# Kernel tuning notes

Hardware: AMD Instinct MI355X
Metric: run time of the kernel (lower is better)

Reference implementation:

```python
import jax, jax.numpy as jnp
import numpy as np

jax.config.update("jax_enable_x64", True)

MAX_LEN = 2048
D_MODEL = 2048
CONTEXT = 1
FUDGE = 0.01
MIN_PERIOD = 1
MAX_PERIOD = 1024
FORGOTTEN_AT = 0.01


def _init_params():
    # Mirrors LaplaceAggregation.__init__ with init_method='linspace', modify_real=True
    limit = np.log(np.finfo(np.float64).max) / MAX_LEN - FUDGE
    soft_high = np.log(FORGOTTEN_AT) / MAX_PERIOD
    soft_low = np.log(FORGOTTEN_AT) / MIN_PERIOD
    a_low = max(-limit + FUDGE, soft_low)
    a_high = max(min(-1e-6, soft_high), a_low)
    a = np.linspace(a_low, a_high, D_MODEL).reshape(1, 1, D_MODEL, CONTEXT)
    b = (2.0 * np.pi / np.linspace(MIN_PERIOD, MAX_PERIOD, D_MODEL)).reshape(1, 1, D_MODEL, CONTEXT)
    return jnp.asarray(a, jnp.float64), jnp.asarray(b, jnp.float64)


def setup_inputs() -> dict:
    key = jax.random.key(0)
    k1, k2, k3 = jax.random.split(key, 3)
    B, T, F = 8, 1024, D_MODEL
    x = jax.random.normal(k1, (B, T, F), dtype=jnp.float32)
    mem_real = jax.random.normal(k2, (B, 1, F, CONTEXT), dtype=jnp.float32)
    mem_imag = jax.random.normal(k3, (B, 1, F, CONTEXT), dtype=jnp.float32)
    a, b = _init_params()
    return {"x": x, "mem_real": mem_real, "mem_imag": mem_imag, "a": a, "b": b}


def reference(x, mem_real, mem_imag, a, b):
    # batched_recurrent_update path (1 < T < max_len)
    T = x.shape[1]
    f64, c128 = jnp.float64, jnp.complex128
    ab = a.astype(f64) + 1j * b.astype(f64)           # [1,1,F,C] complex

    def psi(t):  # t: [T] -> [1,T,F,C]
        return jnp.exp(ab * t.reshape(1, -1, 1, 1))

    # inner_idx[:T] = [max_len-1, ..., max_len-T]; outer_idx = -inner_idx
    inner = jnp.arange(MAX_LEN - 1, MAX_LEN - 1 - T, -1, dtype=f64)
    offset = jnp.arange(1, T + 1, dtype=f64)          # state_offset[:T]

    xc = x.astype(f64)[..., None].astype(c128)        # [B,T,F,1]
    z = jnp.cumsum(psi(inner) * xc, axis=1)           # [B,T,F,C]
    mem0 = (mem_real.astype(f64) + 1j * mem_imag.astype(f64))  # [B,1,F,C]
    out = psi(-inner) * z + mem0 * psi(offset)        # [B,T,F,C]
    return out.astype(jnp.complex64)
```

## Files before the change

kernel.cpp:

```cpp
#include <hip/hip_runtime.h>
#include <math.h>

#define BB 8
#define TT 1024
#define FF 2048
#define F2 1024
#define NCH 64
#define LCH 16
#define F2W 8
#define NFB (F2 / F2W)
#define WGT (NCH * F2W)
#define SCAN_R 6


typedef float vf2 __attribute__((ext_vector_type(2)));

__device__ inline void load_ab2(const void* ap, const void* bp, int f,
                                double2& ab0, double2& ab1) {
    double bd = ((const double*)bp)[0];
    if (bd > 6.0 && bd < 6.6) {
        ab0 = make_double2(((const double*)ap)[f],     ((const double*)bp)[f]);
        ab1 = make_double2(((const double*)ap)[f + 1], ((const double*)bp)[f + 1]);
    } else {
        ab0 = make_double2((double)((const float*)ap)[f],
                           (double)((const float*)bp)[f]);
        ab1 = make_double2((double)((const float*)ap)[f + 1],
                           (double)((const float*)bp)[f + 1]);
    }
}

__device__ inline float2 cis_exp_f(double a, double b, double scale) {
    double m = exp(scale * a);
    double s, c;
    sincos(scale * b, &s, &c);
    return make_float2((float)(m * c), (float)(m * s));
}

__device__ inline float2 cmulf(float2 u, float2 v) {
    return make_float2(fmaf(u.x, v.x, -u.y * v.y), fmaf(u.x, v.y, u.y * v.x));
}
__device__ inline float2 csqf(float2 u) {
    return make_float2(fmaf(u.x, u.x, -u.y * u.y), 2.f * u.x * u.y);
}

__device__ inline void nt_store2(float2* p, float lo, float hi) {
    vf2 v; v.x = lo; v.y = hi;
    __builtin_nontemporal_store(v, reinterpret_cast<vf2*>(p));
}

__global__ void __launch_bounds__(WGT, 4)
k_fused(const float2* __restrict__ x2, const float2* __restrict__ mr2,
        const float2* __restrict__ mi2, const void* __restrict__ a,
        const void* __restrict__ b, float2* __restrict__ out2, size_t limit2) {
    __shared__ float4 sS[2][NCH][F2W];

    int tid = threadIdx.x;
    int f2  = tid & (F2W - 1);
    int c   = tid >> 3;

    int bid = blockIdx.x;
    int swz = ((bid & 7) << 7) + (bid >> 3);
    int fb  = swz & (NFB - 1);
    int bb  = swz >> 7;
    int f2g = fb * F2W + f2;

    size_t base2 = ((size_t)bb * TT + (size_t)c * LCH) * F2 + f2g;
    const float2* xp = x2 + base2;

    float2 xv[LCH];
#pragma unroll
    for (int j = 0; j < LCH; ++j) xv[j] = xp[(size_t)j * F2];

    float2 mem_r = mr2[(size_t)bb * F2 + f2g];
    float2 mem_i = mi2[(size_t)bb * F2 + f2g];

    double2 ab0, ab1;
    load_ab2(a, b, 2 * f2g, ab0, ab1);
    float2 l0 = cis_exp_f(ab0.x, ab0.y, 1.0);
    float2 l1 = cis_exp_f(ab1.x, ab1.y, 1.0);

    float4 z[LCH];
    float zr0 = 0.f, zi0 = 0.f, zr1 = 0.f, zi1 = 0.f;
#pragma unroll
    for (int j = 0; j < LCH; ++j) {
        float2 xvj = xv[j];
        float nr0 = fmaf(l0.x, zr0, fmaf(-l0.y, zi0, xvj.x));
        float ni0 = fmaf(l0.x, zi0, l0.y * zr0);
        float nr1 = fmaf(l1.x, zr1, fmaf(-l1.y, zi1, xvj.y));
        float ni1 = fmaf(l1.x, zi1, l1.y * zr1);
        zr0 = nr0; zi0 = ni0; zr1 = nr1; zi1 = ni1;
        z[j] = make_float4(zr0, zi0, zr1, zi1);
    }

    float2 m0 = l0, m1 = l1;
#pragma unroll
    for (int s = 0; s < 4; ++s) { m0 = csqf(m0); m1 = csqf(m1); }

    float4 P = z[LCH - 1];
    float2 e0 = make_float2(1.f, 0.f), e1 = make_float2(1.f, 0.f);

    sS[0][c][f2] = P;
    __syncthreads();
    int pb = 0;
#pragma unroll
    for (int r = 0; r < SCAN_R; ++r) {
        int k = 1 << r;
        float4 part = make_float4(0.f, 0.f, 0.f, 0.f);
        if (c >= k) part = sS[pb][c - k][f2];
        if ((c >> r) & 1) { e0 = cmulf(e0, m0); e1 = cmulf(e1, m1); }
        P.x = fmaf(m0.x, part.x, fmaf(-m0.y, part.y, P.x));
        P.y = fmaf(m0.x, part.y, fmaf( m0.y, part.x, P.y));
        P.z = fmaf(m1.x, part.z, fmaf(-m1.y, part.w, P.z));
        P.w = fmaf(m1.x, part.w, fmaf( m1.y, part.z, P.w));
        m0 = csqf(m0); m1 = csqf(m1);
        sS[pb ^ 1][c][f2] = P;
        __syncthreads();
        pb ^= 1;
    }
    float4 Pm1 = make_float4(0.f, 0.f, 0.f, 0.f);
    if (c > 0) Pm1 = sS[pb][c - 1][f2];

    float Wr0 = fmaf(e0.x, mem_r.x, fmaf(-e0.y, mem_i.x, Pm1.x));
    float Wi0 = fmaf(e0.x, mem_i.x, fmaf( e0.y, mem_r.x, Pm1.y));
    float Wr1 = fmaf(e1.x, mem_r.y, fmaf(-e1.y, mem_i.y, Pm1.z));
    float Wi1 = fmaf(e1.x, mem_i.y, fmaf( e1.y, mem_r.y, Pm1.w));

    const size_t plane2 = (size_t)BB * TT * F2;
#pragma unroll
    for (int j = 0; j < LCH; ++j) {
        float nWr0 = fmaf(l0.x, Wr0, -l0.y * Wi0);
        float nWi0 = fmaf(l0.x, Wi0,  l0.y * Wr0);
        float nWr1 = fmaf(l1.x, Wr1, -l1.y * Wi1);
        float nWi1 = fmaf(l1.x, Wi1,  l1.y * Wr1);
        Wr0 = nWr0; Wi0 = nWi0; Wr1 = nWr1; Wi1 = nWi1;
        float4 zj = z[j];
        size_t idx2 = base2 + (size_t)j * F2;
        if (idx2 < limit2) nt_store2(&out2[idx2], zj.x + Wr0, zj.z + Wr1);
        size_t ii2 = idx2 + plane2;
        if (ii2 < limit2) nt_store2(&out2[ii2], zj.y + Wi0, zj.w + Wi1);
    }
}

extern "C" void kernel_launch(void* const* d_in, const int* in_sizes, int n_in,
                              void* d_out, int out_size, void* d_ws, size_t ws_size,
                              hipStream_t stream) {
    const float2* x2  = (const float2*)d_in[0];
    const float2* mr2 = (const float2*)d_in[1];
    const float2* mi2 = (const float2*)d_in[2];
    const void*   a   = d_in[3];
    const void*   b   = d_in[4];
    float2* out2 = (float2*)d_out;
    (void)d_ws; (void)ws_size; (void)n_in; (void)in_sizes;

    size_t limit2 = (size_t)out_size >> 1;

    int grid = BB * NFB;
    k_fused<<<grid, WGT, 0, stream>>>(x2, mr2, mi2, a, b, out2, limit2);
}
```

Before: 128.3 us.

## Process four batches per workgroup with register double-buffered prefetch of x

Each workgroup now handles four batch rows for its feature slice, so the grid shrinks by a factor of four. While one tile is computed, the x values for the next batch are prefetched into a second register buffer. The per-chunk decay factor e is now computed directly with exp/sincos instead of being accumulated during the scan, and the per-thread setup (lambda, its powers, e) is amortised across the four tiles. In exchange the kernel uses more registers, launch bounds drop to two workgroups per CU, and the smaller grid exposes less parallelism.

```diff
diff --git a/kernel.cpp b/kernel.cpp
--- a/kernel.cpp
+++ b/kernel.cpp
@@ -11,6 +11,7 @@
 #define NFB (F2 / F2W)
 #define WGT (NCH * F2W)
 #define SCAN_R 6
+#define NTILE 4
 
 
 typedef float vf2 __attribute__((ext_vector_type(2)));
@@ -36,9 +37,6 @@
     return make_float2((float)(m * c), (float)(m * s));
 }
 
-__device__ inline float2 cmulf(float2 u, float2 v) {
-    return make_float2(fmaf(u.x, v.x, -u.y * v.y), fmaf(u.x, v.y, u.y * v.x));
-}
 __device__ inline float2 csqf(float2 u) {
     return make_float2(fmaf(u.x, u.x, -u.y * u.y), 2.f * u.x * u.y);
 }
@@ -48,7 +46,79 @@
     __builtin_nontemporal_store(v, reinterpret_cast<vf2*>(p));
 }
 
-__global__ void __launch_bounds__(WGT, 4)
+#define DO_TILE(XV, XN, BB_CUR, BB_NXT, HAVE_NXT)                              \
+  do {                                                                         \
+        \
+    float2 mem_r = mr2[(size_t)(BB_CUR) * F2 + f2g];                           \
+    float2 mem_i = mi2[(size_t)(BB_CUR) * F2 + f2g];                           \
+                 \
+    if (HAVE_NXT) {                                                            \
+      const float2* xpn =                                                      \
+          x2 + ((size_t)(BB_NXT) * TT + (size_t)c * LCH) * F2 + f2g;           \
+      _Pragma("unroll")                                                        \
+      for (int j = 0; j < LCH; ++j) (XN)[j] = xpn[(size_t)j * F2];             \
+    }                                                                          \
+         \
+    float4 z[LCH];                                                             \
+    {                                                                          \
+      float zr0 = 0.f, zi0 = 0.f, zr1 = 0.f, zi1 = 0.f;                        \
+      _Pragma("unroll")                                                        \
+      for (int j = 0; j < LCH; ++j) {                                          \
+        float2 xvj = (XV)[j];                                                  \
+        float nr0 = fmaf(l0.x, zr0, fmaf(-l0.y, zi0, xvj.x));                  \
+        float ni0 = fmaf(l0.x, zi0, l0.y * zr0);                               \
+        float nr1 = fmaf(l1.x, zr1, fmaf(-l1.y, zi1, xvj.y));                  \
+        float ni1 = fmaf(l1.x, zi1, l1.y * zr1);                               \
+        zr0 = nr0; zi0 = ni0; zr1 = nr1; zi1 = ni1;                            \
+        z[j] = make_float4(zr0, zi0, zr1, zi1);                                \
+      }                                                                        \
+    }                                                                          \
+            \
+    float4 P = z[LCH - 1];                                                     \
+    float2 m0 = m0b, m1 = m1b;                                                 \
+    __syncthreads();           \
+    sS[0][c][f2] = P;                                                          \
+    __syncthreads();                                                           \
+    int pb = 0;                                                                \
+    _Pragma("unroll")                                                          \
+    for (int r = 0; r < SCAN_R; ++r) {                                         \
+      int k = 1 << r;                                                          \
+      float4 part = make_float4(0.f, 0.f, 0.f, 0.f);                           \
+      if (c >= k) part = sS[pb][c - k][f2];                                    \
+      P.x = fmaf(m0.x, part.x, fmaf(-m0.y, part.y, P.x));                      \
+      P.y = fmaf(m0.x, part.y, fmaf( m0.y, part.x, P.y));                      \
+      P.z = fmaf(m1.x, part.z, fmaf(-m1.y, part.w, P.z));                      \
+      P.w = fmaf(m1.x, part.w, fmaf( m1.y, part.z, P.w));                      \
+      m0 = csqf(m0); m1 = csqf(m1);                                            \
+      sS[pb ^ 1][c][f2] = P;                                                   \
+      __syncthreads();                                                         \
+      pb ^= 1;                                                                 \
+    }                                                                          \
+    float4 Pm1 = make_float4(0.f, 0.f, 0.f, 0.f);                              \
+    if (c > 0) Pm1 = sS[pb][c - 1][f2];                                        \
+                                  \
+    float Wr0 = fmaf(e0.x, mem_r.x, fmaf(-e0.y, mem_i.x, Pm1.x));              \
+    float Wi0 = fmaf(e0.x, mem_i.x, fmaf( e0.y, mem_r.x, Pm1.y));              \
+    float Wr1 = fmaf(e1.x, mem_r.y, fmaf(-e1.y, mem_i.y, Pm1.z));              \
+    float Wi1 = fmaf(e1.x, mem_i.y, fmaf( e1.y, mem_r.y, Pm1.w));              \
+                  \
+    size_t base2 = ((size_t)(BB_CUR) * TT + (size_t)c * LCH) * F2 + f2g;       \
+    _Pragma("unroll")                                                          \
+    for (int j = 0; j < LCH; ++j) {                                            \
+      float nWr0 = fmaf(l0.x, Wr0, -l0.y * Wi0);                               \
+      float nWi0 = fmaf(l0.x, Wi0,  l0.y * Wr0);                               \
+      float nWr1 = fmaf(l1.x, Wr1, -l1.y * Wi1);                               \
+      float nWi1 = fmaf(l1.x, Wi1,  l1.y * Wr1);                               \
+      Wr0 = nWr0; Wi0 = nWi0; Wr1 = nWr1; Wi1 = nWi1;                          \
+      float4 zj = z[j];                                                        \
+      size_t idx2 = base2 + (size_t)j * F2;                                    \
+      if (idx2 < limit2) nt_store2(&out2[idx2], zj.x + Wr0, zj.z + Wr1);       \
+      size_t ii2 = idx2 + plane2;                                              \
+      if (ii2 < limit2) nt_store2(&out2[ii2], zj.y + Wi0, zj.w + Wi1);         \
+    }                                                                          \
+  } while (0)
+
+__global__ void __launch_bounds__(WGT, 2)
 k_fused(const float2* __restrict__ x2, const float2* __restrict__ mr2,
         const float2* __restrict__ mi2, const void* __restrict__ a,
         const void* __restrict__ b, float2* __restrict__ out2, size_t limit2) {
@@ -59,86 +129,36 @@
     int c   = tid >> 3;
 
     int bid = blockIdx.x;
-    int swz = ((bid & 7) << 7) + (bid >> 3);
+    int swz = ((bid & 7) << 5) | (bid >> 3);
     int fb  = swz & (NFB - 1);
-    int bb  = swz >> 7;
+    int bq  = swz >> 7;
     int f2g = fb * F2W + f2;
 
-    size_t base2 = ((size_t)bb * TT + (size_t)c * LCH) * F2 + f2g;
-    const float2* xp = x2 + base2;
+    const size_t plane2 = (size_t)BB * TT * F2;
 
-    float2 xv[LCH];
+    int b0 = bq, b1 = bq + 2, b2 = bq + 4, b3 = bq + 6;
+
+    float2 xvA[LCH], xvB[LCH];
+    {
+        const float2* xp0 = x2 + ((size_t)b0 * TT + (size_t)c * LCH) * F2 + f2g;
 #pragma unroll
-    for (int j = 0; j < LCH; ++j) xv[j] = xp[(size_t)j * F2];
-
-    float2 mem_r = mr2[(size_t)bb * F2 + f2g];
-    float2 mem_i = mi2[(size_t)bb * F2 + f2g];
+        for (int j = 0; j < LCH; ++j) xvA[j] = xp0[(size_t)j * F2];
+    }
 
     double2 ab0, ab1;
     load_ab2(a, b, 2 * f2g, ab0, ab1);
     float2 l0 = cis_exp_f(ab0.x, ab0.y, 1.0);
     float2 l1 = cis_exp_f(ab1.x, ab1.y, 1.0);
+    float2 m0b = l0, m1b = l1;
+#pragma unroll
+    for (int s = 0; s < 4; ++s) { m0b = csqf(m0b); m1b = csqf(m1b); }
+    float2 e0 = cis_exp_f(ab0.x, ab0.y, (double)(c * LCH));
+    float2 e1 = cis_exp_f(ab1.x, ab1.y, (double)(c * LCH));
 
-    float4 z[LCH];
-    float zr0 = 0.f, zi0 = 0.f, zr1 = 0.f, zi1 = 0.f;
-#pragma unroll
-    for (int j = 0; j < LCH; ++j) {
-        float2 xvj = xv[j];
-        float nr0 = fmaf(l0.x, zr0, fmaf(-l0.y, zi0, xvj.x));
-        float ni0 = fmaf(l0.x, zi0, l0.y * zr0);
-        float nr1 = fmaf(l1.x, zr1, fmaf(-l1.y, zi1, xvj.y));
-        float ni1 = fmaf(l1.x, zi1, l1.y * zr1);
-        zr0 = nr0; zi0 = ni0; zr1 = nr1; zi1 = ni1;
-        z[j] = make_float4(zr0, zi0, zr1, zi1);
-    }
-
-    float2 m0 = l0, m1 = l1;
-#pragma unroll
-    for (int s = 0; s < 4; ++s) { m0 = csqf(m0); m1 = csqf(m1); }
-
-    float4 P = z[LCH - 1];
-    float2 e0 = make_float2(1.f, 0.f), e1 = make_float2(1.f, 0.f);
-
-    sS[0][c][f2] = P;
-    __syncthreads();
-    int pb = 0;
-#pragma unroll
-    for (int r = 0; r < SCAN_R; ++r) {
-        int k = 1 << r;
-        float4 part = make_float4(0.f, 0.f, 0.f, 0.f);
-        if (c >= k) part = sS[pb][c - k][f2];
-        if ((c >> r) & 1) { e0 = cmulf(e0, m0); e1 = cmulf(e1, m1); }
-        P.x = fmaf(m0.x, part.x, fmaf(-m0.y, part.y, P.x));
-        P.y = fmaf(m0.x, part.y, fmaf( m0.y, part.x, P.y));
-        P.z = fmaf(m1.x, part.z, fmaf(-m1.y, part.w, P.z));
-        P.w = fmaf(m1.x, part.w, fmaf( m1.y, part.z, P.w));
-        m0 = csqf(m0); m1 = csqf(m1);
-        sS[pb ^ 1][c][f2] = P;
-        __syncthreads();
-        pb ^= 1;
-    }
-    float4 Pm1 = make_float4(0.f, 0.f, 0.f, 0.f);
-    if (c > 0) Pm1 = sS[pb][c - 1][f2];
-
-    float Wr0 = fmaf(e0.x, mem_r.x, fmaf(-e0.y, mem_i.x, Pm1.x));
-    float Wi0 = fmaf(e0.x, mem_i.x, fmaf( e0.y, mem_r.x, Pm1.y));
-    float Wr1 = fmaf(e1.x, mem_r.y, fmaf(-e1.y, mem_i.y, Pm1.z));
-    float Wi1 = fmaf(e1.x, mem_i.y, fmaf( e1.y, mem_r.y, Pm1.w));
-
-    const size_t plane2 = (size_t)BB * TT * F2;
-#pragma unroll
-    for (int j = 0; j < LCH; ++j) {
-        float nWr0 = fmaf(l0.x, Wr0, -l0.y * Wi0);
-        float nWi0 = fmaf(l0.x, Wi0,  l0.y * Wr0);
-        float nWr1 = fmaf(l1.x, Wr1, -l1.y * Wi1);
-        float nWi1 = fmaf(l1.x, Wi1,  l1.y * Wr1);
-        Wr0 = nWr0; Wi0 = nWi0; Wr1 = nWr1; Wi1 = nWi1;
-        float4 zj = z[j];
-        size_t idx2 = base2 + (size_t)j * F2;
-        if (idx2 < limit2) nt_store2(&out2[idx2], zj.x + Wr0, zj.z + Wr1);
-        size_t ii2 = idx2 + plane2;
-        if (ii2 < limit2) nt_store2(&out2[ii2], zj.y + Wi0, zj.w + Wi1);
-    }
+    DO_TILE(xvA, xvB, b0, b1, 1);
+    DO_TILE(xvB, xvA, b1, b2, 1);
+    DO_TILE(xvA, xvB, b2, b3, 1);
+    DO_TILE(xvB, xvA, b3, b3, 0);
 }
 
 extern "C" void kernel_launch(void* const* d_in, const int* in_sizes, int n_in,
@@ -154,6 +174,6 @@
 
     size_t limit2 = (size_t)out_size >> 1;
 
-    int grid = BB * NFB;
+    int grid = (BB / NTILE) * NFB;
     k_fused<<<grid, WGT, 0, stream>>>(x2, mr2, mi2, a, b, out2, limit2);
 }
```

Result: no change. 127.1 us (-1.0%).
